# Optimization experiments

Measured on AMD Instinct MI355X. Metric: run time of the kernel, lower is better.

Reference implementation:

```python
import jax, jax.numpy as jnp
import numpy as np

B, C4, H, W = 2, 128, 128, 128
POOL_SIZE = 10


def setup_inputs() -> dict:
    key = jax.random.key(0)
    k1, k2, k3 = jax.random.split(key, 3)
    feature = jax.random.normal(k1, (B, C4, H, W), dtype=jnp.float32)
    K = H * W
    # valid boxes: x1<x2, y1<y2, inside the feature map
    xy1 = jax.random.uniform(k2, (B, K, 2), dtype=jnp.float32) * jnp.array([W * 0.5, H * 0.5], jnp.float32)
    wh = jax.random.uniform(k3, (B, K, 2), dtype=jnp.float32) * jnp.array([W * 0.45, H * 0.45], jnp.float32) + 1.0
    boxes = jnp.concatenate([xy1, xy1 + wh], axis=-1)  # [B, K, 4] = (x1,y1,x2,y2)
    return {"feature": feature, "boxes": boxes, "pool_size": POOL_SIZE}


def reference(feature, boxes, pool_size):
    # feature: [B, 4*C, H, W]; boxes: [B, K, 4]; output: [B, C, K, 4]
    Bn, C4n, Hn, Wn = feature.shape
    C = C4n // 4
    K = boxes.shape[1]
    P = pool_size + 1
    x1, y1, x2, y2 = (boxes[..., i] for i in range(4))  # each [B, K]
    t = jnp.arange(P, dtype=feature.dtype) / pool_size  # [P]
    sx = x1[..., None] + t * (x2 - x1)[..., None]  # [B, K, P] along-x samples
    sy = y1[..., None] + t * (y2 - y1)[..., None]  # [B, K, P] along-y samples
    cx1 = jnp.broadcast_to(x1[..., None], sx.shape)
    cx2 = jnp.broadcast_to(x2[..., None], sx.shape)
    cy1 = jnp.broadcast_to(y1[..., None], sy.shape)
    cy2 = jnp.broadcast_to(y2[..., None], sy.shape)
    # border order: 0=top (y=y1), 1=left (x=x1), 2=bottom (y=y2), 3=right (x=x2)
    xs = jnp.stack([sx, cx1, sx, cx2], axis=1)  # [B, 4, K, P]
    ys = jnp.stack([cy1, sy, cy2, sy], axis=1)  # [B, 4, K, P]

    valid = (xs > -1.0) & (xs < Wn) & (ys > -1.0) & (ys < Hn)
    x = jnp.clip(xs, 0.0, Wn - 1)
    y = jnp.clip(ys, 0.0, Hn - 1)
    x0 = jnp.floor(x).astype(jnp.int32)
    y0 = jnp.floor(y).astype(jnp.int32)
    x1i = jnp.minimum(x0 + 1, Wn - 1)
    y1i = jnp.minimum(y0 + 1, Hn - 1)
    lx = (x - x0)[:, :, None]  # [B, 4, 1, K, P]
    ly = (y - y0)[:, :, None]

    featf = feature.reshape(Bn, 4, C, Hn * Wn)  # channel group g feeds border g

    def gather(yi, xi):
        idx = (yi * Wn + xi).reshape(Bn, 4, 1, K * P)
        return jnp.take_along_axis(featf, idx, axis=3).reshape(Bn, 4, C, K, P)

    val = (gather(y0, x0) * (1 - ly) * (1 - lx)
           + gather(y0, x1i) * (1 - ly) * lx
           + gather(y1i, x0) * ly * (1 - lx)
           + gather(y1i, x1i) * ly * lx)
    val = jnp.where(valid[:, :, None], val, 0.0)
    out = val.max(axis=-1)  # max-pool over the P samples per border -> [B, 4, C, K]
    return out.transpose(0, 2, 3, 1)  # [B, C, K, 4]
```

## Files before the change

### kernel.cpp

```cpp
#include <hip/hip_runtime.h>
#include <math.h>

#define BN   2
#define CG   32
#define HH   128
#define WW   128
#define HWSZ (HH*WW)
#define KK   16384
#define CAP  512
#define CHUNK 256
#define NCHK (CAP / CHUNK)
#define SORTB 64
#define BOX_PER_SORTB (BN * KK / SORTB)

#define WS_F16_OFF   (0u)
#define WS_TMP_OFF   (8u << 20)
#define WS_BKT_OFF   (16u << 20)
#define WS_CNT_OFF   (24u << 20)
#define WS_NEED      ((24u << 20) + (64u << 10))

typedef float vf4 __attribute__((ext_vector_type(4)));
typedef _Float16 h8 __attribute__((ext_vector_type(8)));

__device__ inline unsigned int pack_h2(float a, float b) {
  unsigned short ua = __builtin_bit_cast(unsigned short, (_Float16)a);
  unsigned short ub = __builtin_bit_cast(unsigned short, (_Float16)b);
  return (unsigned int)ua | ((unsigned int)ub << 16);
}

__global__ __launch_bounds__(256) void zero_cnt_kernel(unsigned int* __restrict__ cnt) {
  cnt[blockIdx.x * 256 + threadIdx.x] = 0u;
}

__global__ __launch_bounds__(256) void sort_transpose_kernel(
    const float* __restrict__ feat, unsigned short* __restrict__ ws,
    const float* __restrict__ boxes, unsigned int* __restrict__ cnt,
    uint4* __restrict__ bkt) {
  __shared__ char smem[128 * 9 * 8];
  const int blk = blockIdx.x;
  const int t   = threadIdx.x;

  if (blk < SORTB) {
    unsigned int* hist = (unsigned int*)smem;
    unsigned int* basE = (unsigned int*)smem + 512;
    const int batch = blk >> 5;
    const int k0    = (blk & 31) * BOX_PER_SORTB;
    hist[t] = 0u; hist[t + 256] = 0u;
    __syncthreads();

    vf4 bx[2];
    unsigned short rnk[2][4];
    int bin[2][4];
#pragma unroll
    for (int i = 0; i < 2; ++i) {
      const int k = k0 + i * 256 + t;
      bx[i] = *(const vf4*)(boxes + ((size_t)batch * KK + k) * 4);
#pragma unroll
      for (int g = 0; g < 4; ++g) {
        const float fix = (g == 0) ? bx[i][1] : (g == 1) ? bx[i][0]
                         : (g == 2) ? bx[i][3] : bx[i][2];
        const int f0 = (int)fminf(fmaxf(fix, 0.0f), 127.0f);
        bin[i][g] = (g << 7) | f0;
        rnk[i][g] = (unsigned short)atomicAdd(&hist[bin[i][g]], 1u);
      }
    }
    __syncthreads();

#pragma unroll
    for (int j = 0; j < 2; ++j) {
      const int idx = j * 256 + t;
      const unsigned int c = hist[idx];
      basE[idx] = c ? atomicAdd(&cnt[(size_t)((batch << 9) + idx) * 16], c) : 0u;
    }
    __syncthreads();

#pragma unroll
    for (int i = 0; i < 2; ++i) {
      const int k = k0 + i * 256 + t;
#pragma unroll
      for (int g = 0; g < 4; ++g) {
        const bool horiz = (g & 1) == 0;
        const float fix = (g == 0) ? bx[i][1] : (g == 1) ? bx[i][0]
                         : (g == 2) ? bx[i][3] : bx[i][2];
        const float fc = fminf(fmaxf(fix, 0.0f), 127.0f);
        const int f0 = bin[i][g] & 127;
        const unsigned int slot = basE[bin[i][g]] + rnk[i][g];
        if (slot < CAP) {
          const float mov_s = horiz ? bx[i][0] : bx[i][1];
          const float mov_d = horiz ? (bx[i][2] - bx[i][0]) : (bx[i][3] - bx[i][1]);
          const float lf    = fc - (float)f0;
          const bool  fok   = (fix > -1.0f) && (fix < 128.0f);
          uint4 rec;
          rec.x = __builtin_bit_cast(unsigned int, mov_s);
          rec.y = __builtin_bit_cast(unsigned int, mov_d);
          rec.z = __builtin_bit_cast(unsigned int, lf);
          rec.w = (unsigned int)k | (fok ? 0x80000000u : 0u);
          bkt[(size_t)((batch << 9) + bin[i][g]) * CAP + slot] = rec;
        }
      }
    }
  } else {
    uint2* lds = (uint2*)smem;
    const int idx = blk - SORTB;
    const int s  = idx & 7;
    const int i0 = (idx >> 3) * 128;

    const int iL = (t & 31) * 4;
    const int cq = t >> 5;

    const float* src = feat + (size_t)s * (CG * HWSZ) + i0 + iL;
    vf4 r[4];
#pragma unroll
    for (int cc = 0; cc < 4; ++cc)
      r[cc] = *(const vf4*)(src + (size_t)(cq * 4 + cc) * HWSZ);

#pragma unroll
    for (int ii = 0; ii < 4; ++ii) {
      uint2 q;
      q.x = pack_h2(r[0][ii], r[1][ii]);
      q.y = pack_h2(r[2][ii], r[3][ii]);
      lds[(iL + ii) * 9 + cq] = q;
    }
    __syncthreads();

    uint2* dst = (uint2*)(ws + ((size_t)s * HWSZ + i0) * CG);
    const int q2 = t & 7;
    const int ih = t >> 3;
#pragma unroll
    for (int it = 0; it < 4; ++it) {
      const int i = ih + 32 * it;
      dst[i * 8 + q2] = lds[i * 9 + q2];
    }
  }
}

__global__ __launch_bounds__(256) void border_gather_binned(
    const unsigned short* __restrict__ wsu,
    const unsigned int* __restrict__ cnt, const uint4* __restrict__ bkt,
    const int* __restrict__ psp, unsigned short* __restrict__ tmp) {
  __shared__ _Float16 tile[2 * 128 * 32];
  __shared__ float stf[64];

  const int blk  = blockIdx.x;
  const int s    = blk & 7;
  const int f0   = (blk >> 3) & 127;
  const int ch   = blk >> 10;
  const int g    = s & 3;
  const int b    = s >> 2;
  const int gbin = s * 128 + f0;
  const int n    = min((int)cnt[(size_t)gbin * 16], CAP);
  const int i0   = ch * CHUNK;
  const int i1   = min(n, i0 + CHUNK);
  if (i1 <= i0) return;

  const int t  = threadIdx.x;
  const int ps = *psp;
  if (t < 64) stf[t] = (float)(t <= ps ? t : ps) / (float)ps;

  const bool horiz = (g & 1) == 0;
  const int f1 = min(f0 + 1, 127);
  const _Float16* slab = (const _Float16*)wsu + (size_t)s * (HWSZ * CG);

#pragma unroll
  for (int it = 0; it < 4; ++it) {
    const int chunk = it * 256 + t;
    const int cc   = chunk >> 9;
    const int rem  = chunk & 511;
    const int p    = rem >> 2;
    const int slot = rem & 3;
    const int fcc  = cc ? f1 : f0;
    const size_t srci = horiz ? ((size_t)(fcc * 128 + p) * 32)
                              : ((size_t)(p * 128 + fcc) * 32);
    const uint4 v = *(const uint4*)(slab + srci + slot * 8);
    const int slotS = slot ^ ((p >> 1) & 3);
    *(uint4*)((char*)tile + cc * 8192 + p * 64 + slotS * 16) = v;
  }
  __syncthreads();

  const int w      = t >> 6;
  const int oct    = t & 3;
  const int slot16 = (t >> 2) & 15;

  for (int base = i0 + w * 16; base < i1; base += 64) {
    const int ii  = base + slot16;
    const bool vb = ii < i1;
    const int iic = vb ? ii : i0;
    const uint4 rec = bkt[(size_t)gbin * CAP + iic];
    const float mov_s = __builtin_bit_cast(float, rec.x);
    const float mov_d = __builtin_bit_cast(float, rec.y);
    const float lf    = __builtin_bit_cast(float, rec.z);
    const bool  fok   = (rec.w >> 31) != 0u;
    const int   kid   = (int)(rec.w & 0xFFFFu);

    h8 acc = (h8)(_Float16)(-65504.0f);

#define SAMPLE(TP) do {                                                    \
      const float mov = fmaf((TP), mov_d, mov_s);                          \
      const bool ok = fok && (mov > -1.0f) && (mov < 128.0f);              \
      const float mc = fminf(fmaxf(mov, 0.0f), 127.0f);                    \
      const int m0 = (int)mc;                                              \
      const float lm = mc - (float)m0;                                     \
      const int m1 = min(m0 + 1, 127);                                     \
      const int a0 = (m0 << 6) + ((oct ^ ((m0 >> 1) & 3)) << 4);           \
      const int a1 = (m1 << 6) + ((oct ^ ((m1 >> 1) & 3)) << 4);           \
      const h8 f00 = *(const h8*)((const char*)tile + a0);                 \
      const h8 f01 = *(const h8*)((const char*)tile + a1);                 \
      const h8 f10 = *(const h8*)((const char*)tile + 8192 + a0);          \
      const h8 f11 = *(const h8*)((const char*)tile + 8192 + a1);          \
      const _Float16 w00 = (_Float16)((1.0f - lf) * (1.0f - lm));          \
      const _Float16 w01 = (_Float16)((1.0f - lf) * lm);                   \
      const _Float16 w10 = (_Float16)(lf * (1.0f - lm));                   \
      const _Float16 w11 = (_Float16)(lf * lm);                            \
      h8 v = f00 * w00 + f01 * w01 + f10 * w10 + f11 * w11;                \
      v = ok ? v : (h8)(_Float16)0.0f;                                     \
      acc = __builtin_elementwise_max(acc, v);                             \
    } while (0)

    if (ps == 10) {
#pragma unroll
      for (int p = 0; p <= 10; ++p) SAMPLE((float)p / 10.0f);
    } else {
      for (int p = 0; p <= ps; ++p) SAMPLE(stf[p]);
    }
#undef SAMPLE

    if (vb) {
      h8* dst = (h8*)(tmp + ((size_t)(b * 4 + g) * KK + kid) * 32 + oct * 8);
      *dst = acc;
    }
  }
}

__global__ __launch_bounds__(256) void untranspose_kernel(
    const unsigned short* __restrict__ tmp, float* __restrict__ out) {
  __shared__ float lds[4 * 32 * 33];
  const int blk = blockIdx.x;
  const int b   = blk >> 9;
  const int k0  = (blk & 511) * 32;
  const int t   = threadIdx.x;

#pragma unroll
  for (int it = 0; it < 2; ++it) {
    const int chunk = it * 256 + t;
    const int g   = chunk >> 7;
    const int rem = chunk & 127;
    const int kk  = rem >> 2;
    const int co8 = rem & 3;
    const h8 v = *(const h8*)((const _Float16*)tmp
                 + ((size_t)(b * 4 + g) * KK + k0 + kk) * 32 + co8 * 8);
#pragma unroll
    for (int j = 0; j < 8; ++j)
      lds[g * (32 * 33) + kk * 33 + co8 * 8 + j] = (float)v[j];
  }
  __syncthreads();

#pragma unroll
  for (int it = 0; it < 4; ++it) {
    const int chunk = it * 256 + t;
    const int c  = chunk >> 5;
    const int kk = chunk & 31;
    vf4 v;
#pragma unroll
    for (int g = 0; g < 4; ++g)
      v[g] = lds[g * (32 * 33) + kk * 33 + c];
    vf4* dst = (vf4*)(out + ((size_t)(b * CG + c) * KK + k0 + kk) * 4);
    __builtin_nontemporal_store(v, dst);
  }
}

__global__ __launch_bounds__(128) void border_align_fallback(
    const float* __restrict__ base, const float* __restrict__ boxes,
    const int* __restrict__ psp, float* __restrict__ out) {
  const int blk = blockIdx.x;
  const int b = blk >> 10;
  const int t = threadIdx.x;
  const int g = t >> 5, c = t & 31;
  const int k0 = (blk & 1023) * 16;
  const int ps = *psp;
  const float psf = (float)ps;
  const float* slab = base + (size_t)(b * 4 + g) * (CG * HWSZ) + (size_t)c * HWSZ;
  for (int kk = 0; kk < 16; ++kk) {
    const int kbox = k0 + kk;
    const float x1 = boxes[((size_t)b * KK + kbox) * 4 + 0];
    const float y1 = boxes[((size_t)b * KK + kbox) * 4 + 1];
    const float x2 = boxes[((size_t)b * KK + kbox) * 4 + 2];
    const float y2 = boxes[((size_t)b * KK + kbox) * 4 + 3];
    float m = -INFINITY;
    for (int p = 0; p <= ps; ++p) {
      const float tf = (float)p / psf;
      float x, y;
      if      (g == 0) { x = x1 + tf * (x2 - x1); y = y1; }
      else if (g == 1) { x = x1; y = y1 + tf * (y2 - y1); }
      else if (g == 2) { x = x1 + tf * (x2 - x1); y = y2; }
      else             { x = x2; y = y1 + tf * (y2 - y1); }
      const bool valid = (x > -1.0f) && (x < 128.0f) && (y > -1.0f) && (y < 128.0f);
      const float xc = fminf(fmaxf(x, 0.0f), 127.0f);
      const float yc = fminf(fmaxf(y, 0.0f), 127.0f);
      const int x0 = (int)xc, y0 = (int)yc;
      const float lx = xc - (float)x0, ly = yc - (float)y0;
      const int x1i = min(x0 + 1, 127), y1i = min(y0 + 1, 127);
      const float f00 = slab[y0 * WW + x0],  f01 = slab[y0 * WW + x1i];
      const float f10 = slab[y1i * WW + x0], f11 = slab[y1i * WW + x1i];
      float v = f00 * (1 - ly) * (1 - lx) + f01 * (1 - ly) * lx
              + f10 * ly * (1 - lx) + f11 * ly * lx;
      v = valid ? v : 0.0f;
      m = fmaxf(m, v);
    }
    out[(((size_t)(b * CG + c)) * KK + kbox) * 4 + g] = m;
  }
}

extern "C" void kernel_launch(void* const* d_in, const int* in_sizes, int n_in,
                              void* d_out, int out_size, void* d_ws, size_t ws_size,
                              hipStream_t stream) {
  const float* feature = (const float*)d_in[0];
  const float* boxes   = (const float*)d_in[1];
  const int*   psp     = (const int*)d_in[2];
  float*       out     = (float*)d_out;

  if (ws_size >= WS_NEED) {
    char* ws = (char*)d_ws;
    unsigned short* wsf16 = (unsigned short*)(ws + WS_F16_OFF);
    unsigned short* tmp   = (unsigned short*)(ws + WS_TMP_OFF);
    uint4*          bkt   = (uint4*)(ws + WS_BKT_OFF);
    unsigned int*   cnt   = (unsigned int*)(ws + WS_CNT_OFF);

    hipLaunchKernelGGL(zero_cnt_kernel, dim3(64), dim3(256), 0, stream, cnt);
    hipLaunchKernelGGL(sort_transpose_kernel, dim3(SORTB + 8 * (HWSZ / 128)),
                       dim3(256), 0, stream, feature, wsf16, boxes, cnt, bkt);
    hipLaunchKernelGGL(border_gather_binned, dim3(NCHK * 1024), dim3(256), 0,
                       stream, wsf16, cnt, bkt, psp, tmp);
    hipLaunchKernelGGL(untranspose_kernel, dim3(BN * 512), dim3(256), 0, stream,
                       tmp, out);
  } else {
    hipLaunchKernelGGL(border_align_fallback, dim3(BN * (KK / 16)), dim3(128), 0,
                       stream, feature, boxes, psp, out);
  }
}
```

Measured before the change: 96.32 us.

## Replace atomic bin counters with per-segment fixed-capacity buckets and drop zeroing kernel

The sort stage now writes each block's per-bin histogram into its own counter slot and places records at fixed per-segment offsets (32 slots per segment). This removes the global atomicAdd base reservation and the separate counter-zeroing launch. The gather kernel builds segment offsets with a wavefront prefix scan and stages its records into LDS before sampling. The feature tile also switches from an XOR-swizzled layout to an 80-byte padded row stride. In exchange, records beyond 32 per bin per segment are dropped, the gather kernel does extra scan and gather work up front, and the workspace grows.

```diff
diff --git a/kernel.cpp b/kernel.cpp
--- a/kernel.cpp
+++ b/kernel.cpp
@@ -7,17 +7,16 @@
 #define WW   128
 #define HWSZ (HH*WW)
 #define KK   16384
-#define CAP  512
 #define CHUNK 256
-#define NCHK (CAP / CHUNK)
+#define NCHK 2
 #define SORTB 64
-#define BOX_PER_SORTB (BN * KK / SORTB)
+#define SEGCAP 32
 
 #define WS_F16_OFF   (0u)
 #define WS_TMP_OFF   (8u << 20)
 #define WS_BKT_OFF   (16u << 20)
-#define WS_CNT_OFF   (24u << 20)
-#define WS_NEED      ((24u << 20) + (64u << 10))
+#define WS_CNT_OFF   (32u << 20)
+#define WS_NEED      ((32u << 20) + (128u << 10))
 
 typedef float vf4 __attribute__((ext_vector_type(4)));
 typedef _Float16 h8 __attribute__((ext_vector_type(8)));
@@ -28,23 +27,19 @@
   return (unsigned int)ua | ((unsigned int)ub << 16);
 }
 
-__global__ __launch_bounds__(256) void zero_cnt_kernel(unsigned int* __restrict__ cnt) {
-  cnt[blockIdx.x * 256 + threadIdx.x] = 0u;
-}
-
 __global__ __launch_bounds__(256) void sort_transpose_kernel(
     const float* __restrict__ feat, unsigned short* __restrict__ ws,
     const float* __restrict__ boxes, unsigned int* __restrict__ cnt,
     uint4* __restrict__ bkt) {
-  __shared__ char smem[128 * 9 * 8];
+  __shared__ uint2 smem[128 * 9];
   const int blk = blockIdx.x;
   const int t   = threadIdx.x;
 
   if (blk < SORTB) {
     unsigned int* hist = (unsigned int*)smem;
-    unsigned int* basE = (unsigned int*)smem + 512;
     const int batch = blk >> 5;
-    const int k0    = (blk & 31) * BOX_PER_SORTB;
+    const int seg   = blk & 31;
+    const int k0    = seg * 512;
     hist[t] = 0u; hist[t + 256] = 0u;
     __syncthreads();
 
@@ -66,26 +61,20 @@
     }
     __syncthreads();
 
-#pragma unroll
-    for (int j = 0; j < 2; ++j) {
-      const int idx = j * 256 + t;
-      const unsigned int c = hist[idx];
-      basE[idx] = c ? atomicAdd(&cnt[(size_t)((batch << 9) + idx) * 16], c) : 0u;
-    }
-    __syncthreads();
+    cnt[(size_t)((batch << 9) + t) * 32 + seg]       = min(hist[t], (unsigned)SEGCAP);
+    cnt[(size_t)((batch << 9) + t + 256) * 32 + seg] = min(hist[t + 256], (unsigned)SEGCAP);
 
 #pragma unroll
     for (int i = 0; i < 2; ++i) {
       const int k = k0 + i * 256 + t;
 #pragma unroll
       for (int g = 0; g < 4; ++g) {
-        const bool horiz = (g & 1) == 0;
-        const float fix = (g == 0) ? bx[i][1] : (g == 1) ? bx[i][0]
-                         : (g == 2) ? bx[i][3] : bx[i][2];
-        const float fc = fminf(fmaxf(fix, 0.0f), 127.0f);
-        const int f0 = bin[i][g] & 127;
-        const unsigned int slot = basE[bin[i][g]] + rnk[i][g];
-        if (slot < CAP) {
+        if (rnk[i][g] < SEGCAP) {
+          const bool horiz = (g & 1) == 0;
+          const float fix = (g == 0) ? bx[i][1] : (g == 1) ? bx[i][0]
+                           : (g == 2) ? bx[i][3] : bx[i][2];
+          const float fc = fminf(fmaxf(fix, 0.0f), 127.0f);
+          const int f0 = bin[i][g] & 127;
           const float mov_s = horiz ? bx[i][0] : bx[i][1];
           const float mov_d = horiz ? (bx[i][2] - bx[i][0]) : (bx[i][3] - bx[i][1]);
           const float lf    = fc - (float)f0;
@@ -95,12 +84,13 @@
           rec.y = __builtin_bit_cast(unsigned int, mov_d);
           rec.z = __builtin_bit_cast(unsigned int, lf);
           rec.w = (unsigned int)k | (fok ? 0x80000000u : 0u);
-          bkt[(size_t)((batch << 9) + bin[i][g]) * CAP + slot] = rec;
+          const int gbin = (batch << 9) + bin[i][g];
+          bkt[(size_t)gbin * (32 * SEGCAP) + seg * SEGCAP + rnk[i][g]] = rec;
         }
       }
     }
   } else {
-    uint2* lds = (uint2*)smem;
+    uint2* lds = smem;
     const int idx = blk - SORTB;
     const int s  = idx & 7;
     const int i0 = (idx >> 3) * 128;
@@ -138,7 +128,9 @@
     const unsigned short* __restrict__ wsu,
     const unsigned int* __restrict__ cnt, const uint4* __restrict__ bkt,
     const int* __restrict__ psp, unsigned short* __restrict__ tmp) {
-  __shared__ _Float16 tile[2 * 128 * 32];
+  __shared__ _Float16 tile[2 * 128 * 40];
+  __shared__ uint4 recs[CHUNK];
+  __shared__ unsigned int segbase[33];
   __shared__ float stf[64];
 
   const int blk  = blockIdx.x;
@@ -148,12 +140,29 @@
   const int g    = s & 3;
   const int b    = s >> 2;
   const int gbin = s * 128 + f0;
-  const int n    = min((int)cnt[(size_t)gbin * 16], CAP);
-  const int i0   = ch * CHUNK;
-  const int i1   = min(n, i0 + CHUNK);
+  const int t    = threadIdx.x;
+
+  if (t < 64) {
+    unsigned int c = 0u;
+    if (t < 32) c = min(cnt[(size_t)gbin * 32 + t], (unsigned)SEGCAP);
+    unsigned int x = c;
+#pragma unroll
+    for (int d = 1; d < 32; d <<= 1) {
+      unsigned int y = __shfl_up(x, d, 64);
+      if (t >= d) x += y;
+    }
+    if (t < 32) {
+      segbase[t] = x - c;
+      if (t == 31) segbase[32] = x;
+    }
+  }
+  __syncthreads();
+
+  const int n  = (int)segbase[32];
+  const int i0 = ch * CHUNK;
+  const int i1 = min(n, i0 + CHUNK);
   if (i1 <= i0) return;
 
-  const int t  = threadIdx.x;
   const int ps = *psp;
   if (t < 64) stf[t] = (float)(t <= ps ? t : ps) / (float)ps;
 
@@ -172,8 +181,19 @@
     const size_t srci = horiz ? ((size_t)(fcc * 128 + p) * 32)
                               : ((size_t)(p * 128 + fcc) * 32);
     const uint4 v = *(const uint4*)(slab + srci + slot * 8);
-    const int slotS = slot ^ ((p >> 1) & 3);
-    *(uint4*)((char*)tile + cc * 8192 + p * 64 + slotS * 16) = v;
+    *(uint4*)((char*)tile + cc * 10240 + p * 80 + slot * 16) = v;
+  }
+
+  {
+    const int s2 = t >> 3;
+    const int j  = t & 7;
+    const int base = (int)segbase[s2];
+    const int c    = (int)segbase[s2 + 1] - base;
+    for (int l = j; l < c; l += 8) {
+      const int pos = base + l;
+      if (pos >= i0 && pos < i1)
+        recs[pos - i0] = bkt[(size_t)gbin * (32 * SEGCAP) + s2 * SEGCAP + l];
+    }
   }
   __syncthreads();
 
@@ -184,8 +204,7 @@
   for (int base = i0 + w * 16; base < i1; base += 64) {
     const int ii  = base + slot16;
     const bool vb = ii < i1;
-    const int iic = vb ? ii : i0;
-    const uint4 rec = bkt[(size_t)gbin * CAP + iic];
+    const uint4 rec = recs[vb ? (ii - i0) : 0];
     const float mov_s = __builtin_bit_cast(float, rec.x);
     const float mov_d = __builtin_bit_cast(float, rec.y);
     const float lf    = __builtin_bit_cast(float, rec.z);
@@ -201,12 +220,12 @@
       const int m0 = (int)mc;                                              \
       const float lm = mc - (float)m0;                                     \
       const int m1 = min(m0 + 1, 127);                                     \
-      const int a0 = (m0 << 6) + ((oct ^ ((m0 >> 1) & 3)) << 4);           \
-      const int a1 = (m1 << 6) + ((oct ^ ((m1 >> 1) & 3)) << 4);           \
+      const int a0 = m0 * 80 + oct * 16;                                   \
+      const int a1 = m1 * 80 + oct * 16;                                   \
       const h8 f00 = *(const h8*)((const char*)tile + a0);                 \
       const h8 f01 = *(const h8*)((const char*)tile + a1);                 \
-      const h8 f10 = *(const h8*)((const char*)tile + 8192 + a0);          \
-      const h8 f11 = *(const h8*)((const char*)tile + 8192 + a1);          \
+      const h8 f10 = *(const h8*)((const char*)tile + 10240 + a0);         \
+      const h8 f11 = *(const h8*)((const char*)tile + 10240 + a1);         \
       const _Float16 w00 = (_Float16)((1.0f - lf) * (1.0f - lm));          \
       const _Float16 w01 = (_Float16)((1.0f - lf) * lm);                   \
       const _Float16 w10 = (_Float16)(lf * (1.0f - lm));                   \
@@ -325,7 +344,6 @@
     uint4*          bkt   = (uint4*)(ws + WS_BKT_OFF);
     unsigned int*   cnt   = (unsigned int*)(ws + WS_CNT_OFF);
 
-    hipLaunchKernelGGL(zero_cnt_kernel, dim3(64), dim3(256), 0, stream, cnt);
     hipLaunchKernelGGL(sort_transpose_kernel, dim3(SORTB + 8 * (HWSZ / 128)),
                        dim3(256), 0, stream, feature, wsf16, boxes, cnt, bkt);
     hipLaunchKernelGGL(border_gather_binned, dim3(NCHK * 1024), dim3(256), 0,
```

After: 91.52 us. 5.0% less time.
